# Kernel tuning notes

Hardware: AMD Instinct MI355X
Metric: run time of the kernel (lower is better)

## Reference

```python
import jax, jax.numpy as jnp
import numpy as np

N_NODES = 50000
N_EDGES = 800000
D = 128
BN_EPS = 1e-5
AGG_EPS = 1e-6


def setup_inputs() -> dict:
    key = jax.random.key(0)
    ks = jax.random.split(key, 20)
    s = 1.0 / np.sqrt(D)
    def w(k):
        return jax.random.normal(k, (D, D), jnp.float32) * s
    def b(k):
        return jax.random.normal(k, (D,), jnp.float32) * 0.01
    return {
        "x": jax.random.normal(ks[0], (N_NODES, D), jnp.float32),
        "e": jax.random.normal(ks[1], (N_EDGES, D), jnp.float32),
        "edge_index": jax.random.randint(ks[2], (2, N_EDGES), 0, N_NODES, jnp.int32),
        "WA": w(ks[3]), "bA": b(ks[4]),
        "WB": w(ks[5]), "bB": b(ks[6]),
        "WC": w(ks[7]), "bC": b(ks[8]),
        "WD": w(ks[9]), "bD": b(ks[10]),
        "WE": w(ks[11]), "bE": b(ks[12]),
        "gamma_x": jnp.ones((D,), jnp.float32), "beta_x": jnp.zeros((D,), jnp.float32),
        "gamma_e": jnp.ones((D,), jnp.float32), "beta_e": jnp.zeros((D,), jnp.float32),
    }


def _batchnorm(v, gamma, beta):
    # training-mode BatchNorm1d: batch stats, biased variance
    mean = v.mean(axis=0)
    var = v.var(axis=0)
    return gamma * (v - mean) * jax.lax.rsqrt(var + BN_EPS) + beta


def reference(x, e, edge_index, WA, bA, WB, bB, WC, bC, WD, bD, WE, bE,
              gamma_x, beta_x, gamma_e, beta_e):
    n_nodes = x.shape[0]
    src = edge_index[0]  # x_j (source)
    dst = edge_index[1]  # x_i (target), aggregation index

    Ax = x @ WA + bA
    Bx = x @ WB + bB
    Ce = e @ WC + bC
    Dx = x @ WD + bD
    Ex = x @ WE + bE

    # message: gather endpoints, gate
    e_ij = Dx[dst] + Ex[src] + Ce            # [n_edges, D]
    sigma_ij = jax.nn.sigmoid(e_ij)

    # aggregate: scatter-sum numerator & denominator, normalize
    num = jax.ops.segment_sum(sigma_ij * Bx[src], dst, num_segments=n_nodes)
    den = jax.ops.segment_sum(sigma_ij, dst, num_segments=n_nodes)
    aggr = num / (den + AGG_EPS)

    # update + BN + ReLU (dropout=0, residual=False per GraphGym wrapper)
    x_out = jax.nn.relu(_batchnorm(Ax + aggr, gamma_x, beta_x))
    e_out = jax.nn.relu(_batchnorm(e_ij, gamma_e, beta_e))
    return x_out, e_out
```

## Files before the change

kernel.cpp:

```cpp
#include <hip/hip_runtime.h>
#include <stdint.h>

#define DD 128
#define NB_G 2048
#define GE   2048

using f32x4  = __attribute__((ext_vector_type(4))) float;
using bf16x8 = __attribute__((ext_vector_type(8))) short;

__device__ __forceinline__ float bf2f(short u) {
  union { unsigned int i; float f; } c;
  c.i = ((unsigned int)(unsigned short)u) << 16;
  return c.f;
}
__device__ __forceinline__ short f2bf(float f) {
  union { float f; unsigned int i; } c;
  c.f = f;
  unsigned int u = c.i;
  u += 0x7fffu + ((u >> 16) & 1u);
  return (short)(u >> 16);
}

__global__ __launch_bounds__(256) void k_prep(
    const float* __restrict__ WA, const float* __restrict__ WB, const float* __restrict__ WC,
    const float* __restrict__ WD, const float* __restrict__ WE,
    short* __restrict__ WtA, short* __restrict__ WtB, short* __restrict__ WtC,
    short* __restrict__ WtD, short* __restrict__ WtE,
    int* __restrict__ deg, int n) {
  int t = threadIdx.x;
  if (blockIdx.x < 5) {
    const float* Ws[5] = {WA, WB, WC, WD, WE};
    short* Os[5] = {WtA, WtB, WtC, WtD, WtE};
    const float* W = Ws[blockIdx.x];
    short* O = Os[blockIdx.x];
    int c = t & 127, h = t >> 7;
    for (int p = 0; p < 8; ++p) {
      int k0 = (h * 8 + p) * 8;
      bf16x8 v;
      #pragma unroll
      for (int j = 0; j < 8; ++j) v[j] = f2bf(W[(size_t)(k0 + j) * DD + c]);
      *(bf16x8*)&O[(size_t)c * DD + k0] = v;
    }
  } else {
    int i = (blockIdx.x - 5) * 256 + t;
    if (i < n) deg[i] = 0;
  }
}

__global__ __launch_bounds__(256) void k_hist(const int* __restrict__ dst, int* __restrict__ deg, int E) {
  int e = blockIdx.x * 256 + threadIdx.x;
  if (e < E) atomicAdd(&deg[dst[e]], 1);
}

__global__ __launch_bounds__(256) void k_scan1(const int* __restrict__ deg, int* __restrict__ off,
                                               int* __restrict__ totals, int n) {
  __shared__ int sm[256];
  int t = threadIdx.x;
  int i = blockIdx.x * 256 + t;
  int v = (i < n) ? deg[i] : 0;
  sm[t] = v;
  __syncthreads();
  int acc = v;
  #pragma unroll
  for (int d = 1; d < 256; d <<= 1) {
    int add = (t >= d) ? sm[t - d] : 0;
    __syncthreads();
    acc += add;
    sm[t] = acc;
    __syncthreads();
  }
  if (i < n) off[i] = acc - v;
  if (t == 255) totals[blockIdx.x] = acc;
}

__global__ __launch_bounds__(256) void k_scan2(const int* __restrict__ totals, int* __restrict__ boff, int nb) {
  __shared__ int sm[256];
  int t = threadIdx.x;
  int v = (t < nb) ? totals[t] : 0;
  sm[t] = v;
  __syncthreads();
  int acc = v;
  #pragma unroll
  for (int d = 1; d < 256; d <<= 1) {
    int add = (t >= d) ? sm[t - d] : 0;
    __syncthreads();
    acc += add;
    sm[t] = acc;
    __syncthreads();
  }
  boff[t] = acc - v;
}

__global__ __launch_bounds__(256) void k_scan3(int* __restrict__ off, const int* __restrict__ boff,
                                               int* __restrict__ cursor, int n) {
  int i = blockIdx.x * 256 + threadIdx.x;
  if (i < n) {
    int o = off[i] + boff[blockIdx.x];
    off[i] = o;
    cursor[i] = o;
  }
}

__global__ __launch_bounds__(256) void k_fill(const int* __restrict__ dst, const int* __restrict__ src,
                                              int* __restrict__ cursor, int* __restrict__ list,
                                              int* __restrict__ srcS, int* __restrict__ posOf, int E) {
  int e = blockIdx.x * 256 + threadIdx.x;
  if (e < E) {
    int p = atomicAdd(&cursor[dst[e]], 1);
    list[p] = e;
    srcS[p] = src[e];
    posOf[e] = p;
  }
}

__global__ __launch_bounds__(256) void k_nodegemm(
    const float* __restrict__ x,
    const short* __restrict__ WtA, const float* __restrict__ bA,
    const short* __restrict__ WtB, const float* __restrict__ bB,
    const short* __restrict__ WtD, const float* __restrict__ bD,
    const short* __restrict__ WtE, const float* __restrict__ bE,
    short* __restrict__ Axh, short* __restrict__ Bxh,
    short* __restrict__ Dxh, short* __restrict__ Exh, int n) {
  int t = threadIdx.x;
  int w = t >> 6, l = t & 63, lg = l >> 4, lc = l & 15;
  int m0 = blockIdx.x * 64;
  int row = m0 + w * 16 + lc;
  bool valid = row < n;
  int rowc = valid ? row : n - 1;

  const float* xr = x + (size_t)rowc * DD;
  bf16x8 af[4];
  #pragma unroll
  for (int kk = 0; kk < 4; ++kk) {
    float4 a0 = *(const float4*)&xr[kk * 32 + lg * 8];
    float4 a1 = *(const float4*)&xr[kk * 32 + lg * 8 + 4];
    af[kk][0] = f2bf(a0.x); af[kk][1] = f2bf(a0.y); af[kk][2] = f2bf(a0.z); af[kk][3] = f2bf(a0.w);
    af[kk][4] = f2bf(a1.x); af[kk][5] = f2bf(a1.y); af[kk][6] = f2bf(a1.z); af[kk][7] = f2bf(a1.w);
  }

  const short* Wt[4] = {WtA, WtB, WtD, WtE};
  const float* bs[4] = {bA, bB, bD, bE};
  short* Os[4] = {Axh, Bxh, Dxh, Exh};

  #pragma unroll
  for (int mi = 0; mi < 4; ++mi) {
    const short* Wm = Wt[mi];
    f32x4 acc[8] = {};
    #pragma unroll
    for (int kk = 0; kk < 4; ++kk) {
      #pragma unroll
      for (int tt = 0; tt < 8; ++tt) {
        bf16x8 bfv = *(const bf16x8*)&Wm[(size_t)(tt * 16 + lc) * DD + kk * 32 + lg * 8];
        acc[tt] = __builtin_amdgcn_mfma_f32_16x16x32_bf16(bfv, af[kk], acc[tt], 0, 0, 0);
      }
    }
    if (valid) {
      short* O = Os[mi];
      #pragma unroll
      for (int tt = 0; tt < 8; ++tt) {
        int f0 = tt * 16 + lg * 4;
        float4 bc = *(const float4*)&bs[mi][f0];
        short4 o;
        o.x = f2bf(acc[tt][0] + bc.x);
        o.y = f2bf(acc[tt][1] + bc.y);
        o.z = f2bf(acc[tt][2] + bc.z);
        o.w = f2bf(acc[tt][3] + bc.w);
        *(short4*)&O[(size_t)row * DD + f0] = o;
      }
    }
  }
}

__global__ __launch_bounds__(256) void k_edge(
    const float* __restrict__ e, const short* __restrict__ WtC, const float* __restrict__ bC,
    const int* __restrict__ srcI, const int* __restrict__ dstI, const int* __restrict__ posOf,
    const short* __restrict__ Dxh, const short* __restrict__ Exh,
    short* __restrict__ eijS, float* __restrict__ pE, int Etot, int ntiles) {
  __shared__ __align__(16) short lds_wt[32 * 64 * 8];
  __shared__ __align__(16) short es[4][16][136];
  int t = threadIdx.x;
  int w = t >> 6, l = t & 63, lg = l >> 4, lc = l & 15;

  #pragma unroll
  for (int i = 0; i < 8; ++i) {
    int slot = w * 8 + i;
    int tt = slot >> 2, kk = slot & 3;
    bf16x8 v = *(const bf16x8*)&WtC[(size_t)(tt * 16 + lc) * DD + kk * 32 + lg * 8];
    *(bf16x8*)&lds_wt[(slot * 64 + l) * 8] = v;
  }
  __syncthreads();

  float bCv[8];
  #pragma unroll
  for (int tt = 0; tt < 8; ++tt) bCv[tt] = bC[tt * 16 + lc];

  float se[8] = {}, qe[8] = {};

  const int stride = gridDim.x;
  int tile = blockIdx.x;

  float4 e32[8];
  int dnN[4], snN[4], posN[4];

  {
    size_t m0 = (size_t)tile * 64;
    size_t row = m0 + w * 16 + lc;
    if (row >= (size_t)Etot) row = Etot - 1;
    const float* er = e + row * DD;
    #pragma unroll
    for (int kk = 0; kk < 4; ++kk) {
      e32[kk * 2]     = *(const float4*)&er[kk * 32 + lg * 8];
      e32[kk * 2 + 1] = *(const float4*)&er[kk * 32 + lg * 8 + 4];
    }
    #pragma unroll
    for (int z = 0; z < 4; ++z) {
      size_t erow = m0 + w * 16 + z * 4 + lg;
      if (erow >= (size_t)Etot) erow = Etot - 1;
      dnN[z] = dstI[erow]; snN[z] = srcI[erow]; posN[z] = posOf[erow];
    }
  }

  for (; tile < ntiles; tile += stride) {
    int dn[4], sn[4], pos[4];
    #pragma unroll
    for (int z = 0; z < 4; ++z) { dn[z] = dnN[z]; sn[z] = snN[z]; pos[z] = posN[z]; }

    bf16x8 dv[4], sv[4];
    #pragma unroll
    for (int z = 0; z < 4; ++z) {
      dv[z] = *(const bf16x8*)&Dxh[(size_t)dn[z] * DD + lc * 8];
      sv[z] = *(const bf16x8*)&Exh[(size_t)sn[z] * DD + lc * 8];
    }

    bf16x8 af[4];
    #pragma unroll
    for (int kk = 0; kk < 4; ++kk) {
      float4 a0 = e32[kk * 2], a1 = e32[kk * 2 + 1];
      af[kk][0] = f2bf(a0.x); af[kk][1] = f2bf(a0.y); af[kk][2] = f2bf(a0.z); af[kk][3] = f2bf(a0.w);
      af[kk][4] = f2bf(a1.x); af[kk][5] = f2bf(a1.y); af[kk][6] = f2bf(a1.z); af[kk][7] = f2bf(a1.w);
    }

    int nt = tile + stride;
    if (nt < ntiles) {
      size_t m0n = (size_t)nt * 64;
      size_t row = m0n + w * 16 + lc;
      if (row >= (size_t)Etot) row = Etot - 1;
      const float* er = e + row * DD;
      #pragma unroll
      for (int kk = 0; kk < 4; ++kk) {
        e32[kk * 2]     = *(const float4*)&er[kk * 32 + lg * 8];
        e32[kk * 2 + 1] = *(const float4*)&er[kk * 32 + lg * 8 + 4];
      }
      #pragma unroll
      for (int z = 0; z < 4; ++z) {
        size_t erow = m0n + w * 16 + z * 4 + lg;
        if (erow >= (size_t)Etot) erow = Etot - 1;
        dnN[z] = dstI[erow]; snN[z] = srcI[erow]; posN[z] = posOf[erow];
      }
    }

    f32x4 acc[8] = {};
    #pragma unroll
    for (int kk = 0; kk < 4; ++kk) {
      #pragma unroll
      for (int tt = 0; tt < 8; ++tt) {
        bf16x8 bfv = *(const bf16x8*)&lds_wt[((tt * 4 + kk) * 64 + l) * 8];
        acc[tt] = __builtin_amdgcn_mfma_f32_16x16x32_bf16(af[kk], bfv, acc[tt], 0, 0, 0);
      }
    }

    #pragma unroll
    for (int tt = 0; tt < 8; ++tt) {
      int col = tt * 16 + lc;
      #pragma unroll
      for (int j = 0; j < 4; ++j)
        es[w][lg * 4 + j][col] = f2bf(acc[tt][j] + bCv[tt]);
    }
    asm volatile("s_waitcnt lgkmcnt(0)" ::: "memory");
    __builtin_amdgcn_sched_barrier(0);

    size_t m0 = (size_t)tile * 64;
    #pragma unroll
    for (int z = 0; z < 4; ++z) {
      size_t erow = m0 + w * 16 + z * 4 + lg;
      if (erow < (size_t)Etot) {
        int r = z * 4 + lg;
        bf16x8 cv = *(const bf16x8*)&es[w][r][lc * 8];
        bf16x8 o;
        #pragma unroll
        for (int j = 0; j < 8; ++j) {
          float v = bf2f(cv[j]) + bf2f(dv[z][j]) + bf2f(sv[z][j]);
          se[j] += v; qe[j] += v * v;
          o[j] = f2bf(v);
        }
        *(bf16x8*)&eijS[(size_t)pos[z] * DD + lc * 8] = o;
      }
    }
    __builtin_amdgcn_sched_barrier(0);
  }

  #pragma unroll
  for (int j = 0; j < 8; ++j) {
    se[j] += __shfl_xor(se[j], 16); se[j] += __shfl_xor(se[j], 32);
    qe[j] += __shfl_xor(qe[j], 16); qe[j] += __shfl_xor(qe[j], 32);
  }
  if (lg == 0) {
    size_t base = ((size_t)blockIdx.x * 4 + w) * 256;
    #pragma unroll
    for (int j = 0; j < 8; ++j) {
      pE[base + lc * 8 + j] = se[j];
      pE[base + 128 + lc * 8 + j] = qe[j];
    }
  }
}

__device__ __forceinline__ void proc_edge(int id, bf16x8 ev, bf16x8 bv,
                                          const float* su, const float* hu,
                                          float* num, float* den,
                                          float* __restrict__ oute, int fi) {
  float va[8];
  #pragma unroll
  for (int j = 0; j < 8; ++j) {
    float v0 = bf2f(ev[j]);
    va[j] = fmaxf(0.f, v0 * su[j] + hu[j]);
    float g0 = 1.f / (1.f + __expf(-v0));
    num[j] += g0 * bf2f(bv[j]);
    den[j] += g0;
  }
  float4 oa, ob;
  oa.x = va[0]; oa.y = va[1]; oa.z = va[2]; oa.w = va[3];
  ob.x = va[4]; ob.y = va[5]; ob.z = va[6]; ob.w = va[7];
  *(float4*)&oute[(size_t)id * DD + fi * 8] = oa;
  *(float4*)&oute[(size_t)id * DD + fi * 8 + 4] = ob;
}

__global__ __launch_bounds__(256) void k_gather(
    const int* __restrict__ off, const int* __restrict__ deg, const int* __restrict__ list,
    const int* __restrict__ srcS, const short* __restrict__ eijS, const short* __restrict__ Bxh,
    const short* __restrict__ Axh, const float* __restrict__ stE,
    short* __restrict__ outxh, float* __restrict__ oute,
    float* __restrict__ pX, int n) {
  int t = threadIdx.x;
  int w = t >> 6, l = t & 63;
  int qw = l >> 4, fi = l & 15;
  int waveId = blockIdx.x * 4 + w;
  const int nwaves = NB_G * 4;

  float su[8], hu[8];
  {
    float4 s0 = *(const float4*)&stE[fi * 8], s1 = *(const float4*)&stE[fi * 8 + 4];
    float4 h0 = *(const float4*)&stE[128 + fi * 8], h1 = *(const float4*)&stE[128 + fi * 8 + 4];
    su[0] = s0.x; su[1] = s0.y; su[2] = s0.z; su[3] = s0.w;
    su[4] = s1.x; su[5] = s1.y; su[6] = s1.z; su[7] = s1.w;
    hu[0] = h0.x; hu[1] = h0.y; hu[2] = h0.z; hu[3] = h0.w;
    hu[4] = h1.x; hu[5] = h1.y; hu[6] = h1.z; hu[7] = h1.w;
  }

  float sx[4] = {}, qx[4] = {};
  int c0 = fi * 8 + ((qw & 1) * 4);

  int startC = 0, dgC = 0;
  if (waveId < n) { startC = off[waveId]; dgC = deg[waveId]; }

  for (int node = waveId; node < n; node += nwaves) {
    int start = startC, dg = dgC;
    int nn = node + nwaves;
    if (nn < n) { startC = off[nn]; dgC = deg[nn]; }
    short4 ax = *(const short4*)&Axh[(size_t)node * DD + (qw < 2 ? c0 : fi * 8)];

    float num[8] = {}, den[8] = {};
    int k = qw;
    for (; k + 12 < dg; k += 16) {
      int p0 = start + k, p1 = p0 + 4, p2 = p0 + 8, p3 = p0 + 12;
      int id0 = list[p0], id1 = list[p1], id2 = list[p2], id3 = list[p3];
      int s0 = srcS[p0], s1 = srcS[p1], s2 = srcS[p2], s3 = srcS[p3];
      bf16x8 e0 = *(const bf16x8*)&eijS[(size_t)p0 * DD + fi * 8];
      bf16x8 e1 = *(const bf16x8*)&eijS[(size_t)p1 * DD + fi * 8];
      bf16x8 e2 = *(const bf16x8*)&eijS[(size_t)p2 * DD + fi * 8];
      bf16x8 e3 = *(const bf16x8*)&eijS[(size_t)p3 * DD + fi * 8];
      bf16x8 b0 = *(const bf16x8*)&Bxh[(size_t)s0 * DD + fi * 8];
      bf16x8 b1 = *(const bf16x8*)&Bxh[(size_t)s1 * DD + fi * 8];
      bf16x8 b2 = *(const bf16x8*)&Bxh[(size_t)s2 * DD + fi * 8];
      bf16x8 b3 = *(const bf16x8*)&Bxh[(size_t)s3 * DD + fi * 8];
      proc_edge(id0, e0, b0, su, hu, num, den, oute, fi);
      proc_edge(id1, e1, b1, su, hu, num, den, oute, fi);
      proc_edge(id2, e2, b2, su, hu, num, den, oute, fi);
      proc_edge(id3, e3, b3, su, hu, num, den, oute, fi);
    }
    for (; k + 4 < dg; k += 8) {
      int p0 = start + k, p1 = p0 + 4;
      int id0 = list[p0], id1 = list[p1];
      int s0 = srcS[p0], s1 = srcS[p1];
      bf16x8 e0 = *(const bf16x8*)&eijS[(size_t)p0 * DD + fi * 8];
      bf16x8 e1 = *(const bf16x8*)&eijS[(size_t)p1 * DD + fi * 8];
      bf16x8 b0 = *(const bf16x8*)&Bxh[(size_t)s0 * DD + fi * 8];
      bf16x8 b1 = *(const bf16x8*)&Bxh[(size_t)s1 * DD + fi * 8];
      proc_edge(id0, e0, b0, su, hu, num, den, oute, fi);
      proc_edge(id1, e1, b1, su, hu, num, den, oute, fi);
    }
    for (; k < dg; k += 4) {
      int p0 = start + k;
      int id0 = list[p0];
      int s0 = srcS[p0];
      bf16x8 e0 = *(const bf16x8*)&eijS[(size_t)p0 * DD + fi * 8];
      bf16x8 b0 = *(const bf16x8*)&Bxh[(size_t)s0 * DD + fi * 8];
      proc_edge(id0, e0, b0, su, hu, num, den, oute, fi);
    }
    #pragma unroll
    for (int j = 0; j < 8; ++j) {
      num[j] += __shfl_xor(num[j], 16); num[j] += __shfl_xor(num[j], 32);
      den[j] += __shfl_xor(den[j], 16); den[j] += __shfl_xor(den[j], 32);
    }
    if (qw < 2) {
      short axa[4] = {ax.x, ax.y, ax.z, ax.w};
      short4 o;
      short ov[4];
      #pragma unroll
      for (int j = 0; j < 4; ++j) {
        int jj = qw * 4 + j;
        float aggr = num[jj] / (den[jj] + 1e-6f);
        float xp = bf2f(axa[j]) + aggr;
        ov[j] = f2bf(xp);
        sx[j] += xp; qx[j] += xp * xp;
      }
      o.x = ov[0]; o.y = ov[1]; o.z = ov[2]; o.w = ov[3];
      *(short4*)&outxh[(size_t)node * DD + c0] = o;
    }
  }

  __shared__ float lsX[4][128], lqX[4][128];
  if (qw < 2) {
    #pragma unroll
    for (int j = 0; j < 4; ++j) { lsX[w][fi * 8 + qw * 4 + j] = sx[j]; lqX[w][fi * 8 + qw * 4 + j] = qx[j]; }
  }
  __syncthreads();
  if (t < 128) {
    float a = lsX[0][t] + lsX[1][t] + lsX[2][t] + lsX[3][t];
    float b = lqX[0][t] + lqX[1][t] + lqX[2][t] + lqX[3][t];
    pX[(size_t)blockIdx.x * 256 + t] = a;
    pX[(size_t)blockIdx.x * 256 + 128 + t] = b;
  }
}

__global__ __launch_bounds__(256) void k_reduce(const float* __restrict__ part, int nblk, float invcnt,
                                                const float* __restrict__ gamma, const float* __restrict__ beta,
                                                float* __restrict__ stats) {
  int c = blockIdx.x, t = threadIdx.x;
  float a = 0.f, b = 0.f;
  for (int k = t; k < nblk; k += 256) {
    a += part[(size_t)k * 256 + c];
    b += part[(size_t)k * 256 + 128 + c];
  }
  #pragma unroll
  for (int o = 32; o > 0; o >>= 1) { a += __shfl_down(a, o); b += __shfl_down(b, o); }
  __shared__ float ra[4], rb[4];
  int l = t & 63, w = t >> 6;
  if (l == 0) { ra[w] = a; rb[w] = b; }
  __syncthreads();
  if (t == 0) {
    a = ra[0] + ra[1] + ra[2] + ra[3];
    b = rb[0] + rb[1] + rb[2] + rb[3];
    float mean = a * invcnt;
    float var = b * invcnt - mean * mean;
    float istd = rsqrtf(var + 1e-5f);
    float scale = gamma[c] * istd;
    stats[c] = scale;
    stats[128 + c] = beta[c] - mean * scale;
  }
}

__global__ __launch_bounds__(256) void k_xfinal(const short* __restrict__ vh, const float* __restrict__ st,
                                                float* __restrict__ out, size_t n8) {
  size_t i = (size_t)blockIdx.x * 256 + threadIdx.x;
  if (i >= n8) return;
  bf16x8 u = *(const bf16x8*)&vh[i * 8];
  int f0 = (int)((i * 8) & 127);
  float4 s0 = *(const float4*)&st[f0], s1 = *(const float4*)&st[f0 + 4];
  float4 h0 = *(const float4*)&st[128 + f0], h1 = *(const float4*)&st[128 + f0 + 4];
  float4 a, b;
  a.x = fmaxf(0.f, bf2f(u[0]) * s0.x + h0.x);
  a.y = fmaxf(0.f, bf2f(u[1]) * s0.y + h0.y);
  a.z = fmaxf(0.f, bf2f(u[2]) * s0.z + h0.z);
  a.w = fmaxf(0.f, bf2f(u[3]) * s0.w + h0.w);
  b.x = fmaxf(0.f, bf2f(u[4]) * s1.x + h1.x);
  b.y = fmaxf(0.f, bf2f(u[5]) * s1.y + h1.y);
  b.z = fmaxf(0.f, bf2f(u[6]) * s1.z + h1.z);
  b.w = fmaxf(0.f, bf2f(u[7]) * s1.w + h1.w);
  *(float4*)&out[i * 8] = a;
  *(float4*)&out[i * 8 + 4] = b;
}

extern "C" void kernel_launch(void* const* d_in, const int* in_sizes, int n_in,
                              void* d_out, int out_size, void* d_ws, size_t ws_size,
                              hipStream_t stream) {
  const float* x  = (const float*)d_in[0];
  const float* e  = (const float*)d_in[1];
  const int*   ei = (const int*)d_in[2];
  const float* WA = (const float*)d_in[3];  const float* bA = (const float*)d_in[4];
  const float* WB = (const float*)d_in[5];  const float* bB = (const float*)d_in[6];
  const float* WC = (const float*)d_in[7];  const float* bC = (const float*)d_in[8];
  const float* WD = (const float*)d_in[9];  const float* bD = (const float*)d_in[10];
  const float* WE = (const float*)d_in[11]; const float* bE = (const float*)d_in[12];
  const float* gx = (const float*)d_in[13]; const float* bx = (const float*)d_in[14];
  const float* ge = (const float*)d_in[15]; const float* be = (const float*)d_in[16];

  int N = in_sizes[0] / DD;
  int E = in_sizes[2] / 2;
  const int* srcI = ei;
  const int* dstI = ei + E;

  float* outx = (float*)d_out;
  float* oute = (float*)d_out + (size_t)N * DD;

  int ntilesE = (E + 63) / 64;

  char* wp = (char*)d_ws;
  auto alloc = [&](size_t sz) { char* p = wp; wp += (sz + 255) & ~(size_t)255; return p; };
  short* Axh    = (short*)alloc((size_t)N * DD * 2);
  short* Bxh    = (short*)alloc((size_t)N * DD * 2);
  short* Dxh    = (short*)alloc((size_t)N * DD * 2);
  short* Exh    = (short*)alloc((size_t)N * DD * 2);
  short* eijS   = (short*)alloc((size_t)E * DD * 2);
  short* outxh  = (short*)alloc((size_t)N * DD * 2);
  int*   deg    = (int*)alloc((size_t)N * 4);
  int*   off    = (int*)alloc((size_t)N * 4);
  int*   cursor = (int*)alloc((size_t)N * 4);
  int*   totals = (int*)alloc(1024);
  int*   boff   = (int*)alloc(1024);
  int*   list   = (int*)alloc((size_t)E * 4);
  int*   srcS   = (int*)alloc((size_t)E * 4);
  int*   posOf  = (int*)alloc((size_t)E * 4);
  float* pE     = (float*)alloc((size_t)GE * 4 * 256 * 4);
  float* pX     = (float*)alloc((size_t)NB_G * 256 * 4);
  float* statsE = (float*)alloc(1024);
  float* statsX = (float*)alloc(1024);
  short* WtA    = (short*)alloc((size_t)DD * DD * 2);
  short* WtB    = (short*)alloc((size_t)DD * DD * 2);
  short* WtC    = (short*)alloc((size_t)DD * DD * 2);
  short* WtD    = (short*)alloc((size_t)DD * DD * 2);
  short* WtE    = (short*)alloc((size_t)DD * DD * 2);
  (void)ws_size; (void)n_in; (void)out_size;

  int nsb = (N + 255) / 256;

  k_prep<<<5 + nsb, 256, 0, stream>>>(WA, WB, WC, WD, WE, WtA, WtB, WtC, WtD, WtE, deg, N);
  k_hist<<<(E + 255) / 256, 256, 0, stream>>>(dstI, deg, E);
  k_scan1<<<nsb, 256, 0, stream>>>(deg, off, totals, N);
  k_scan2<<<1, 256, 0, stream>>>(totals, boff, nsb);
  k_scan3<<<nsb, 256, 0, stream>>>(off, boff, cursor, N);
  k_fill<<<(E + 255) / 256, 256, 0, stream>>>(dstI, srcI, cursor, list, srcS, posOf, E);

  k_nodegemm<<<(N + 63) / 64, 256, 0, stream>>>(x, WtA, bA, WtB, bB, WtD, bD, WtE, bE,
                                                Axh, Bxh, Dxh, Exh, N);
  k_edge<<<GE, 256, 0, stream>>>(e, WtC, bC, srcI, dstI, posOf, Dxh, Exh, eijS, pE, E, ntilesE);
  k_reduce<<<128, 256, 0, stream>>>(pE, GE * 4, 1.0f / (float)E, ge, be, statsE);

  k_gather<<<NB_G, 256, 0, stream>>>(off, deg, list, srcS, eijS, Bxh, Axh, statsE,
                                     outxh, oute, pX, N);
  k_reduce<<<128, 256, 0, stream>>>(pX, NB_G, 1.0f / (float)N, gx, bx, statsX);
  k_xfinal<<<(int)(((size_t)N * DD / 8 + 255) / 256), 256, 0, stream>>>(outxh, statsX, outx, (size_t)N * DD / 8);
}
```

Before: 567.0 us.

## Prefetch edge gathers one tile ahead and restructure BN stat reductions

The edge kernel now issues the Dx/Ex row gathers for the next tile at the end of the current iteration, so their latency overlaps the MFMA work of the following tile. The BN partial-sum reduction is split into two kernels: the first has 128 blocks reading rows contiguously, and a single block then finalizes scale and shift. The old version had strided column-wise reads in which each block walked a whole column. The prefetch raises register pressure, and the new reduction adds an extra launch per stats pass.

```diff
diff --git a/kernel.cpp b/kernel.cpp
--- a/kernel.cpp
+++ b/kernel.cpp
@@ -4,6 +4,7 @@
 #define DD 128
 #define NB_G 2048
 #define GE   2048
+#define RB   128
 
 using f32x4  = __attribute__((ext_vector_type(4))) float;
 using bf16x8 = __attribute__((ext_vector_type(8))) short;
@@ -201,6 +202,8 @@
 
   float4 e32[8];
   int dnN[4], snN[4], posN[4];
+  int posC[4];
+  bf16x8 dv[4], sv[4];
 
   {
     size_t m0 = (size_t)tile * 64;
@@ -218,19 +221,16 @@
       if (erow >= (size_t)Etot) erow = Etot - 1;
       dnN[z] = dstI[erow]; snN[z] = srcI[erow]; posN[z] = posOf[erow];
     }
+    #pragma unroll
+    for (int z = 0; z < 4; ++z) {
+      dv[z] = *(const bf16x8*)&Dxh[(size_t)dnN[z] * DD + lc * 8];
+      sv[z] = *(const bf16x8*)&Exh[(size_t)snN[z] * DD + lc * 8];
+      posC[z] = posN[z];
+    }
   }
 
   for (; tile < ntiles; tile += stride) {
-    int dn[4], sn[4], pos[4];
-    #pragma unroll
-    for (int z = 0; z < 4; ++z) { dn[z] = dnN[z]; sn[z] = snN[z]; pos[z] = posN[z]; }
-
-    bf16x8 dv[4], sv[4];
-    #pragma unroll
-    for (int z = 0; z < 4; ++z) {
-      dv[z] = *(const bf16x8*)&Dxh[(size_t)dn[z] * DD + lc * 8];
-      sv[z] = *(const bf16x8*)&Exh[(size_t)sn[z] * DD + lc * 8];
-    }
+    int nt = tile + stride;
 
     bf16x8 af[4];
     #pragma unroll
@@ -240,7 +240,6 @@
       af[kk][4] = f2bf(a1.x); af[kk][5] = f2bf(a1.y); af[kk][6] = f2bf(a1.z); af[kk][7] = f2bf(a1.w);
     }
 
-    int nt = tile + stride;
     if (nt < ntiles) {
       size_t m0n = (size_t)nt * 64;
       size_t row = m0n + w * 16 + lc;
@@ -293,10 +292,19 @@
           se[j] += v; qe[j] += v * v;
           o[j] = f2bf(v);
         }
-        *(bf16x8*)&eijS[(size_t)pos[z] * DD + lc * 8] = o;
+        *(bf16x8*)&eijS[(size_t)posC[z] * DD + lc * 8] = o;
       }
     }
     __builtin_amdgcn_sched_barrier(0);
+
+    if (nt < ntiles) {
+      #pragma unroll
+      for (int z = 0; z < 4; ++z) {
+        dv[z] = *(const bf16x8*)&Dxh[(size_t)dnN[z] * DD + lc * 8];
+        sv[z] = *(const bf16x8*)&Exh[(size_t)snN[z] * DD + lc * 8];
+        posC[z] = posN[z];
+      }
+    }
   }
 
   #pragma unroll
@@ -442,30 +450,30 @@
   }
 }
 
-__global__ __launch_bounds__(256) void k_reduce(const float* __restrict__ part, int nblk, float invcnt,
-                                                const float* __restrict__ gamma, const float* __restrict__ beta,
-                                                float* __restrict__ stats) {
-  int c = blockIdx.x, t = threadIdx.x;
-  float a = 0.f, b = 0.f;
-  for (int k = t; k < nblk; k += 256) {
-    a += part[(size_t)k * 256 + c];
-    b += part[(size_t)k * 256 + 128 + c];
-  }
-  #pragma unroll
-  for (int o = 32; o > 0; o >>= 1) { a += __shfl_down(a, o); b += __shfl_down(b, o); }
-  __shared__ float ra[4], rb[4];
-  int l = t & 63, w = t >> 6;
-  if (l == 0) { ra[w] = a; rb[w] = b; }
+__global__ __launch_bounds__(256) void k_red1(const float* __restrict__ part, int nblk,
+                                              float* __restrict__ pp) {
+  int t = threadIdx.x;
+  float acc = 0.f;
+  for (int k = blockIdx.x; k < nblk; k += gridDim.x)
+    acc += part[(size_t)k * 256 + t];
+  pp[(size_t)blockIdx.x * 256 + t] = acc;
+}
+__global__ __launch_bounds__(256) void k_red2(const float* __restrict__ pp, int nb, float invcnt,
+                                              const float* __restrict__ gamma, const float* __restrict__ beta,
+                                              float* __restrict__ stats) {
+  int t = threadIdx.x;
+  float a = 0.f;
+  for (int b = 0; b < nb; ++b) a += pp[(size_t)b * 256 + t];
+  __shared__ float sm[256];
+  sm[t] = a;
   __syncthreads();
-  if (t == 0) {
-    a = ra[0] + ra[1] + ra[2] + ra[3];
-    b = rb[0] + rb[1] + rb[2] + rb[3];
-    float mean = a * invcnt;
-    float var = b * invcnt - mean * mean;
+  if (t < 128) {
+    float mean = sm[t] * invcnt;
+    float var = sm[128 + t] * invcnt - mean * mean;
     float istd = rsqrtf(var + 1e-5f);
-    float scale = gamma[c] * istd;
-    stats[c] = scale;
-    stats[128 + c] = beta[c] - mean * scale;
+    float scale = gamma[t] * istd;
+    stats[t] = scale;
+    stats[128 + t] = beta[t] - mean * scale;
   }
 }
 
@@ -532,6 +540,8 @@
   int*   posOf  = (int*)alloc((size_t)E * 4);
   float* pE     = (float*)alloc((size_t)GE * 4 * 256 * 4);
   float* pX     = (float*)alloc((size_t)NB_G * 256 * 4);
+  float* ppE    = (float*)alloc((size_t)RB * 256 * 4);
+  float* ppX    = (float*)alloc((size_t)RB * 256 * 4);
   float* statsE = (float*)alloc(1024);
   float* statsX = (float*)alloc(1024);
   short* WtA    = (short*)alloc((size_t)DD * DD * 2);
@@ -553,10 +563,12 @@
   k_nodegemm<<<(N + 63) / 64, 256, 0, stream>>>(x, WtA, bA, WtB, bB, WtD, bD, WtE, bE,
                                                 Axh, Bxh, Dxh, Exh, N);
   k_edge<<<GE, 256, 0, stream>>>(e, WtC, bC, srcI, dstI, posOf, Dxh, Exh, eijS, pE, E, ntilesE);
-  k_reduce<<<128, 256, 0, stream>>>(pE, GE * 4, 1.0f / (float)E, ge, be, statsE);
+  k_red1<<<RB, 256, 0, stream>>>(pE, GE * 4, ppE);
+  k_red2<<<1, 256, 0, stream>>>(ppE, RB, 1.0f / (float)E, ge, be, statsE);
 
   k_gather<<<NB_G, 256, 0, stream>>>(off, deg, list, srcS, eijS, Bxh, Axh, statsE,
                                      outxh, oute, pX, N);
-  k_reduce<<<128, 256, 0, stream>>>(pX, NB_G, 1.0f / (float)N, gx, bx, statsX);
+  k_red1<<<RB, 256, 0, stream>>>(pX, NB_G, ppX);
+  k_red2<<<1, 256, 0, stream>>>(ppX, RB, 1.0f / (float)N, gx, bx, statsX);
   k_xfinal<<<(int)(((size_t)N * DD / 8 + 255) / 256), 256, 0, stream>>>(outxh, statsX, outx, (size_t)N * DD / 8);
 }
```

New measurement: 627.4 us. 10.7% more time.
